# Kernel tuning notes

Hardware: AMD Instinct MI355X
Metric: run time of the kernel (lower is better)

Reference implementation:

```python
import jax, jax.numpy as jnp
import numpy as np

N_NODES = 100000
IN_DIM = 128
HID = 128
N_REL = 2
N_EDGES = 500000


def setup_inputs() -> dict:
    key = jax.random.key(0)
    ks = jax.random.split(key, 12)
    x = jax.random.normal(ks[0], (N_NODES, IN_DIM), dtype=jnp.float32)
    edge_index = jax.random.randint(ks[1], (2, N_EDGES), 0, N_NODES, dtype=jnp.int64)
    edge_type = jax.random.randint(ks[2], (N_EDGES,), 0, N_REL, dtype=jnp.int64)
    def w(k, shape, fan_in):
        return jax.random.normal(k, shape, dtype=jnp.float32) / np.sqrt(fan_in)
    return {
        "x": x,
        "edge_index": edge_index,
        "edge_type": edge_type,
        "W_rel1": w(ks[3], (N_REL, IN_DIM, HID), IN_DIM),
        "W_root1": w(ks[4], (IN_DIM, HID), IN_DIM),
        "b1": jnp.zeros((HID,), jnp.float32),
        "W_rel2": w(ks[5], (N_REL, HID, HID), HID),
        "W_root2": w(ks[6], (HID, HID), HID),
        "b2": jnp.zeros((HID,), jnp.float32),
        "Wc": w(ks[7], (HID, 2), HID),
        "bc": jnp.zeros((2,), jnp.float32),
    }


def rgcn_conv(x, src, dst, edge_type, W_rel, W_root, b, n_nodes):
    """PyG RGCNConv: out_i = x_i @ W_root + b + sum_r mean_{j in N_r(i)} x_j @ W_r."""
    out = x @ W_root + b
    for r in range(W_rel.shape[0]):  # small fixed relation count
        mask = (edge_type == r).astype(x.dtype)  # [E]
        xr = x @ W_rel[r]                         # [N, dout] transform-then-gather
        msg = xr[src] * mask[:, None]             # [E, dout]
        agg = jax.ops.segment_sum(msg, dst, num_segments=n_nodes)   # [N, dout]
        cnt = jax.ops.segment_sum(mask, dst, num_segments=n_nodes)  # [N]
        out = out + agg / jnp.maximum(cnt, 1.0)[:, None]            # mean aggr
    return out


def reference(x, edge_index, edge_type, W_rel1, W_root1, b1, W_rel2, W_root2, b2, Wc, bc):
    n = x.shape[0]
    src, dst = edge_index[0], edge_index[1]
    h = rgcn_conv(x, src, dst, edge_type, W_rel1, W_root1, b1, n)
    h = jax.nn.relu(h)
    # dropout is identity at inference (training=False)
    h = rgcn_conv(h, src, dst, edge_type, W_rel2, W_root2, b2, n)
    h = jax.nn.relu(h)
    logits = h @ Wc + bc
    return logits
```

## Files before the change

kernel.cpp:

```cpp
#include <hip/hip_runtime.h>
#include <hip/hip_fp16.h>

#define N_NODES 100000
#define PAD_N   100096
#define IN_DIM 128
#define HID 128
#define N_REL 2
#define N_EDGES 500000
#define M_SEG (N_REL * N_NODES)
#define SCAN_BLK 1024
#define SCAN_NB ((M_SEG + SCAN_BLK - 1) / SCAN_BLK)

#define CVT_BLOCKS 12500
#define PACK_BLOCKS 48
#define HIST_BLOCKS 1954

typedef __attribute__((ext_vector_type(8))) _Float16 half8;
typedef __attribute__((ext_vector_type(4))) float float4v;

__device__ __forceinline__ unsigned short f2h(float f) {
    return __half_as_ushort(__float2half(f));
}

__global__ __launch_bounds__(256) void prep_kernel(
    const float* __restrict__ X, unsigned short* __restrict__ Xb,
    const float* __restrict__ Wroot1, const float* __restrict__ Wrel1,
    const float* __restrict__ Wroot2, const float* __restrict__ Wrel2,
    unsigned short* __restrict__ Wp,
    const int* __restrict__ ei, const int* __restrict__ et,
    unsigned* __restrict__ cnt)
{
    int bid = blockIdx.x;
    if (bid < CVT_BLOCKS) {
        int i = bid * 256 + threadIdx.x;
        if (i >= N_NODES * IN_DIM / 4) return;
        float4 v = ((const float4*)X)[i];
        ushort4 o;
        o.x = f2h(v.x); o.y = f2h(v.y); o.z = f2h(v.z); o.w = f2h(v.w);
        ((ushort4*)Xb)[i] = o;
    } else if (bid < CVT_BLOCKS + PACK_BLOCKS) {
        int tid = (bid - CVT_BLOCKS) * 256 + threadIdx.x;
        int layer = tid / 6144;
        int rem   = tid % 6144;
        int ks    = rem / 512;
        int rem2  = rem % 512;
        int nt    = rem2 / 64;
        int lane  = rem2 % 64;
        int seg = ks >> 2;
        int kl  = (ks & 3) * 32 + (lane >> 4) * 8;
        int chan = nt * 16 + (lane & 15);
        const float* Wroot = layer ? Wroot2 : Wroot1;
        const float* Wrel  = layer ? Wrel2  : Wrel1;
        const float* W = (seg == 0) ? Wroot : (Wrel + (size_t)(seg - 1) * 128 * 128);
        unsigned short* dst = Wp + (size_t)tid * 8;
        #pragma unroll
        for (int j = 0; j < 8; ++j)
            dst[j] = f2h(W[(size_t)(kl + j) * 128 + chan]);
    } else {
        int e = (bid - CVT_BLOCKS - PACK_BLOCKS) * 256 + threadIdx.x;
        if (e >= N_EDGES) return;
        int dst = ei[N_EDGES + e];
        int r = et[e];
        atomicAdd(cnt + (size_t)r * N_NODES + dst, 1u);
    }
}

__global__ __launch_bounds__(256) void scan1_kernel(
    const unsigned* __restrict__ cnt,
    unsigned* __restrict__ rs, unsigned* __restrict__ bsums)
{
    __shared__ unsigned sdata[256];
    int t = threadIdx.x;
    int base = blockIdx.x * SCAN_BLK + t * 4;
    unsigned v[4]; unsigned s = 0;
    #pragma unroll
    for (int j = 0; j < 4; ++j) {
        v[j] = (base + j < M_SEG) ? cnt[base + j] : 0u;
        s += v[j];
    }
    sdata[t] = s;
    __syncthreads();
    #pragma unroll
    for (int off = 1; off < 256; off <<= 1) {
        unsigned x = (t >= off) ? sdata[t - off] : 0u;
        __syncthreads();
        if (t >= off) sdata[t] += x;
        __syncthreads();
    }
    unsigned excl = (t > 0) ? sdata[t - 1] : 0u;
    if (t == 255) bsums[blockIdx.x] = sdata[255];
    unsigned run = excl;
    #pragma unroll
    for (int j = 0; j < 4; ++j) {
        if (base + j < M_SEG) rs[base + j] = run;
        run += v[j];
    }
}

__global__ __launch_bounds__(256) void scan2_kernel(unsigned* __restrict__ bsums)
{
    __shared__ unsigned sdata[256];
    int t = threadIdx.x;
    sdata[t] = (t < SCAN_NB) ? bsums[t] : 0u;
    __syncthreads();
    #pragma unroll
    for (int off = 1; off < 256; off <<= 1) {
        unsigned x = (t >= off) ? sdata[t - off] : 0u;
        __syncthreads();
        if (t >= off) sdata[t] += x;
        __syncthreads();
    }
    if (t < SCAN_NB) bsums[t] = (t > 0) ? sdata[t - 1] : 0u;
}

__global__ __launch_bounds__(256) void scan3_kernel(
    unsigned* __restrict__ rs, const unsigned* __restrict__ bsums,
    unsigned* __restrict__ cursor)
{
    int i = blockIdx.x * blockDim.x + threadIdx.x;
    if (i < M_SEG) {
        unsigned v = rs[i] + bsums[i >> 10];
        rs[i] = v;
        cursor[i] = v;
    }
    if (i == 0) rs[M_SEG] = N_EDGES;
}

__global__ __launch_bounds__(256) void fill_kernel(
    const int* __restrict__ ei, const int* __restrict__ et,
    unsigned* __restrict__ cursor, unsigned* __restrict__ csr)
{
    int e = blockIdx.x * blockDim.x + threadIdx.x;
    if (e >= N_EDGES) return;
    int src = ei[e];
    int dst = ei[N_EDGES + e];
    int r = et[e];
    unsigned pos = atomicAdd(cursor + (size_t)r * N_NODES + dst, 1u);
    csr[pos] = (unsigned)src;
}

template <bool FINAL>
__global__ __launch_bounds__(256) void gemm_kernel(
    const unsigned short* __restrict__ Xin,
    const unsigned* __restrict__ rs,
    const unsigned* __restrict__ csr,
    const unsigned short* __restrict__ Wp,
    const float* __restrict__ bias,
    unsigned short* __restrict__ Hout,
    const float* __restrict__ Wc,
    const float* __restrict__ bc,
    float* __restrict__ Out)
{
    __shared__ unsigned short ldsB[2][3 * 8 * 512];

    const int t    = threadIdx.x;
    const int w    = t >> 6;
    const int lane = t & 63;
    const int l15  = lane & 15;
    const int quad = lane >> 4;
    const int rowbase = blockIdx.x * 128 + w * 32;
    const int koff = quad * 8;

    auto stage = [&](int ph, int buf) {
        #pragma unroll
        for (int fi = 0; fi < 6; ++fi) {
            int f  = fi * 4 + w;
            int sl = f >> 3;
            int nt = f & 7;
            int ks = ph * 3 + sl;
            const unsigned short* g = Wp + ((size_t)(ks * 8 + nt) * 64 + lane) * 8;
            unsigned short* l = &ldsB[buf][(size_t)(sl * 8 + nt) * 512];
            __builtin_amdgcn_global_load_lds(
                (const __attribute__((address_space(1))) unsigned int*)g,
                (__attribute__((address_space(3))) unsigned int*)l, 16, 0, 0);
        }
    };

    stage(0, 0);

    const uint4* __restrict__ X4 = (const uint4*)Xin;

    half8 ax[2][4];
    #pragma unroll
    for (int mt = 0; mt < 2; ++mt)
        #pragma unroll
        for (int ksl = 0; ksl < 4; ++ksl)
            ax[mt][ksl] = *(const half8*)(Xin +
                (size_t)(rowbase + mt * 16 + l15) * 128 + ksl * 32 + koff);

    half8 ag[2][2][4];
    #pragma unroll
    for (int r = 0; r < 2; ++r) {
        #pragma unroll
        for (int mt = 0; mt < 2; ++mt) {
            int node = rowbase + mt * 16 + l15;
            unsigned start = 0, end = 0;
            if (node < N_NODES) {
                unsigned sg = (unsigned)r * N_NODES + (unsigned)node;
                start = rs[sg];
                end   = rs[sg + 1];
            }
            __half2 a2[4][4];
            #pragma unroll
            for (int ksl = 0; ksl < 4; ++ksl)
                #pragma unroll
                for (int j = 0; j < 4; ++j)
                    a2[ksl][j] = __float2half2_rn(0.f);

            for (unsigned p = start; p < end; ++p) {
                unsigned s = csr[p];
                const uint4* row = X4 + ((size_t)s << 4) + quad;
                uint4 v0 = row[0];
                uint4 v1 = row[4];
                uint4 v2 = row[8];
                uint4 v3 = row[12];
                a2[0][0] = __hadd2(a2[0][0], *(const __half2*)&v0.x);
                a2[0][1] = __hadd2(a2[0][1], *(const __half2*)&v0.y);
                a2[0][2] = __hadd2(a2[0][2], *(const __half2*)&v0.z);
                a2[0][3] = __hadd2(a2[0][3], *(const __half2*)&v0.w);
                a2[1][0] = __hadd2(a2[1][0], *(const __half2*)&v1.x);
                a2[1][1] = __hadd2(a2[1][1], *(const __half2*)&v1.y);
                a2[1][2] = __hadd2(a2[1][2], *(const __half2*)&v1.z);
                a2[1][3] = __hadd2(a2[1][3], *(const __half2*)&v1.w);
                a2[2][0] = __hadd2(a2[2][0], *(const __half2*)&v2.x);
                a2[2][1] = __hadd2(a2[2][1], *(const __half2*)&v2.y);
                a2[2][2] = __hadd2(a2[2][2], *(const __half2*)&v2.z);
                a2[2][3] = __hadd2(a2[2][3], *(const __half2*)&v2.w);
                a2[3][0] = __hadd2(a2[3][0], *(const __half2*)&v3.x);
                a2[3][1] = __hadd2(a2[3][1], *(const __half2*)&v3.y);
                a2[3][2] = __hadd2(a2[3][2], *(const __half2*)&v3.z);
                a2[3][3] = __hadd2(a2[3][3], *(const __half2*)&v3.w);
            }

            unsigned c = end - start;
            float scf = 1.0f / (float)(c > 0u ? c : 1u);
            __half2 s2 = __float2half2_rn(scf);
            #pragma unroll
            for (int ksl = 0; ksl < 4; ++ksl) {
                half8 h;
                #pragma unroll
                for (int j = 0; j < 4; ++j)
                    ((__half2*)&h)[j] = __hmul2(a2[ksl][j], s2);
                ag[r][mt][ksl] = h;
            }
        }
    }

    auto af = [&](int ks, int mt) -> half8 {
        return (ks < 4) ? ax[mt][ks & 3] : ag[(ks >> 2) - 1][mt][ks & 3];
    };

    float4v acc[2][8];
    #pragma unroll
    for (int nt = 0; nt < 8; ++nt) {
        float bv = bias[nt * 16 + l15];
        #pragma unroll
        for (int mt = 0; mt < 2; ++mt)
            acc[mt][nt] = float4v{bv, bv, bv, bv};
    }

    __syncthreads();

    #pragma unroll
    for (int ph = 0; ph < 4; ++ph) {
        if (ph < 3) stage(ph + 1, (ph + 1) & 1);
        #pragma unroll
        for (int sl = 0; sl < 3; ++sl) {
            int ks = ph * 3 + sl;
            half8 b[8];
            #pragma unroll
            for (int nt = 0; nt < 8; ++nt)
                b[nt] = *(const half8*)(&ldsB[ph & 1][(size_t)(sl * 8 + nt) * 512] + lane * 8);
            #pragma unroll
            for (int nt = 0; nt < 8; ++nt) {
                acc[0][nt] = __builtin_amdgcn_mfma_f32_16x16x32_f16(af(ks, 0), b[nt], acc[0][nt], 0, 0, 0);
                acc[1][nt] = __builtin_amdgcn_mfma_f32_16x16x32_f16(af(ks, 1), b[nt], acc[1][nt], 0, 0, 0);
            }
        }
        __syncthreads();
    }

    if (!FINAL) {
        #pragma unroll
        for (int mt = 0; mt < 2; ++mt) {
            #pragma unroll
            for (int r = 0; r < 4; ++r) {
                int node = rowbase + mt * 16 + quad * 4 + r;
                unsigned short* hp = Hout + (size_t)node * 128 + l15;
                #pragma unroll
                for (int nt = 0; nt < 8; ++nt)
                    hp[nt * 16] = f2h(fmaxf(acc[mt][nt][r], 0.f));
            }
        }
    } else {
        float wc0[8], wc1[8];
        #pragma unroll
        for (int nt = 0; nt < 8; ++nt) {
            wc0[nt] = Wc[(nt * 16 + l15) * 2 + 0];
            wc1[nt] = Wc[(nt * 16 + l15) * 2 + 1];
        }
        float b0 = bc[0], b1 = bc[1];
        #pragma unroll
        for (int mt = 0; mt < 2; ++mt) {
            #pragma unroll
            for (int r = 0; r < 4; ++r) {
                float l0 = 0.f, l1 = 0.f;
                #pragma unroll
                for (int nt = 0; nt < 8; ++nt) {
                    float h = fmaxf(acc[mt][nt][r], 0.f);
                    l0 += h * wc0[nt];
                    l1 += h * wc1[nt];
                }
                #pragma unroll
                for (int off = 8; off > 0; off >>= 1) {
                    l0 += __shfl_down(l0, off, 16);
                    l1 += __shfl_down(l1, off, 16);
                }
                int node = rowbase + mt * 16 + quad * 4 + r;
                if (l15 == 0 && node < N_NODES) {
                    Out[(size_t)node * 2 + 0] = l0 + b0;
                    Out[(size_t)node * 2 + 1] = l1 + b1;
                }
            }
        }
    }
}

extern "C" void kernel_launch(void* const* d_in, const int* in_sizes, int n_in,
                              void* d_out, int out_size, void* d_ws, size_t ws_size,
                              hipStream_t stream)
{
    const float* x      = (const float*)d_in[0];
    const int*   ei     = (const int*)d_in[1];
    const int*   et     = (const int*)d_in[2];
    const float* Wrel1  = (const float*)d_in[3];
    const float* Wroot1 = (const float*)d_in[4];
    const float* b1     = (const float*)d_in[5];
    const float* Wrel2  = (const float*)d_in[6];
    const float* Wroot2 = (const float*)d_in[7];
    const float* b2     = (const float*)d_in[8];
    const float* Wc     = (const float*)d_in[9];
    const float* bc     = (const float*)d_in[10];
    float* out = (float*)d_out;

    char* ws = (char*)d_ws;
    size_t off = 0;
    auto alloc = [&](size_t bytes) {
        void* p = ws + off;
        off += (bytes + 255) & ~(size_t)255;
        return p;
    };
    unsigned short* xb    = (unsigned short*)alloc((size_t)PAD_N * IN_DIM * 2);
    unsigned short* h1b   = (unsigned short*)alloc((size_t)PAD_N * HID * 2);
    unsigned short* Wp    = (unsigned short*)alloc((size_t)2 * 12 * 8 * 64 * 8 * 2);
    unsigned*       rs    = (unsigned*)alloc((size_t)(M_SEG + 1) * 4);
    unsigned*       cursor= (unsigned*)alloc((size_t)M_SEG * 4);
    unsigned*       bsums = (unsigned*)alloc(256 * 4);
    unsigned*       csr   = (unsigned*)alloc((size_t)N_EDGES * 4);

    const int edge_blocks = (N_EDGES + 255) / 256;
    const int seg_blocks  = (M_SEG + 255) / 256;
    const int gemm_blocks = PAD_N / 128;
    const int prep_blocks = CVT_BLOCKS + PACK_BLOCKS + HIST_BLOCKS;

    hipMemsetAsync(cursor, 0, (size_t)M_SEG * 4, stream);
    prep_kernel<<<prep_blocks, 256, 0, stream>>>(
        x, xb, Wroot1, Wrel1, Wroot2, Wrel2, Wp, ei, et, cursor);
    scan1_kernel<<<SCAN_NB, 256, 0, stream>>>(cursor, rs, bsums);
    scan2_kernel<<<1, 256, 0, stream>>>(bsums);
    scan3_kernel<<<seg_blocks, 256, 0, stream>>>(rs, bsums, cursor);
    fill_kernel<<<edge_blocks, 256, 0, stream>>>(ei, et, cursor, csr);

    gemm_kernel<false><<<gemm_blocks, 256, 0, stream>>>(
        xb, rs, csr, Wp, b1, h1b, nullptr, nullptr, nullptr);

    gemm_kernel<true><<<gemm_blocks, 256, 0, stream>>>(
        h1b, rs, csr, Wp + (size_t)12 * 8 * 64 * 8, b2, nullptr, Wc, bc, out);
}
```

Before: 273.3 us.

## Interleave four neighbor gathers per lane and load weights directly from global

The neighbor aggregation now advances all four (relation, row-tile) segments together in one predicated loop. Each lane therefore issues four independent row gathers per iteration instead of walking each segment serially, which raises memory-level parallelism. The shared-memory staging of the weight matrix and its block barriers are removed; B and A fragments are loaded straight from global memory into registers with software double buffering. This frees LDS and drops the syncs, but adds register pressure and redundant global weight reads across waves, and masked iterations still issue gathers to row 0.

After: 271.3 us. No clear change (-0.7%).

```diff
diff --git a/kernel.cpp b/kernel.cpp
--- a/kernel.cpp
+++ b/kernel.cpp
@@ -151,8 +151,6 @@
     const float* __restrict__ bc,
     float* __restrict__ Out)
 {
-    __shared__ unsigned short ldsB[2][3 * 8 * 512];
-
     const int t    = threadIdx.x;
     const int w    = t >> 6;
     const int lane = t & 63;
@@ -161,93 +159,98 @@
     const int rowbase = blockIdx.x * 128 + w * 32;
     const int koff = quad * 8;
 
-    auto stage = [&](int ph, int buf) {
-        #pragma unroll
-        for (int fi = 0; fi < 6; ++fi) {
-            int f  = fi * 4 + w;
-            int sl = f >> 3;
-            int nt = f & 7;
-            int ks = ph * 3 + sl;
-            const unsigned short* g = Wp + ((size_t)(ks * 8 + nt) * 64 + lane) * 8;
-            unsigned short* l = &ldsB[buf][(size_t)(sl * 8 + nt) * 512];
-            __builtin_amdgcn_global_load_lds(
-                (const __attribute__((address_space(1))) unsigned int*)g,
-                (__attribute__((address_space(3))) unsigned int*)l, 16, 0, 0);
-        }
-    };
-
-    stage(0, 0);
-
     const uint4* __restrict__ X4 = (const uint4*)Xin;
 
-    half8 ax[2][4];
-    #pragma unroll
-    for (int mt = 0; mt < 2; ++mt)
-        #pragma unroll
-        for (int ksl = 0; ksl < 4; ++ksl)
-            ax[mt][ksl] = *(const half8*)(Xin +
-                (size_t)(rowbase + mt * 16 + l15) * 128 + ksl * 32 + koff);
-
-    half8 ag[2][2][4];
+    unsigned p_[4], e_[4]; float inv_[4];
     #pragma unroll
     for (int r = 0; r < 2; ++r) {
         #pragma unroll
         for (int mt = 0; mt < 2; ++mt) {
+            int c = r * 2 + mt;
             int node = rowbase + mt * 16 + l15;
-            unsigned start = 0, end = 0;
+            unsigned st = 0, en = 0;
             if (node < N_NODES) {
                 unsigned sg = (unsigned)r * N_NODES + (unsigned)node;
-                start = rs[sg];
-                end   = rs[sg + 1];
-            }
-            __half2 a2[4][4];
+                st = rs[sg];
+                en = rs[sg + 1];
+            }
+            p_[c] = st; e_[c] = en;
+            unsigned cdeg = en - st;
+            inv_[c] = 1.0f / (float)(cdeg > 0u ? cdeg : 1u);
+        }
+    }
+
+    __half2 a2[4][4][4];
+    #pragma unroll
+    for (int c = 0; c < 4; ++c)
+        #pragma unroll
+        for (int ksl = 0; ksl < 4; ++ksl)
+            #pragma unroll
+            for (int j = 0; j < 4; ++j)
+                a2[c][ksl][j] = __float2half2_rn(0.f);
+
+    const __half2 one2  = __float2half2_rn(1.f);
+    const __half2 zero2 = __float2half2_rn(0.f);
+
+    while (true) {
+        bool act[4];
+        bool anyl = false;
+        #pragma unroll
+        for (int c = 0; c < 4; ++c) { act[c] = p_[c] < e_[c]; anyl |= act[c]; }
+        if (!__any(anyl)) break;
+
+        unsigned s_[4];
+        #pragma unroll
+        for (int c = 0; c < 4; ++c)
+            s_[c] = csr[act[c] ? p_[c] : 0u];
+
+        uint4 v_[4][4];
+        #pragma unroll
+        for (int c = 0; c < 4; ++c) {
+            const uint4* row = X4 + ((size_t)(act[c] ? s_[c] : 0u) << 4) + quad;
+            v_[c][0] = row[0];
+            v_[c][1] = row[4];
+            v_[c][2] = row[8];
+            v_[c][3] = row[12];
+        }
+
+        #pragma unroll
+        for (int c = 0; c < 4; ++c) {
+            __half2 m = act[c] ? one2 : zero2;
             #pragma unroll
             for (int ksl = 0; ksl < 4; ++ksl)
                 #pragma unroll
                 for (int j = 0; j < 4; ++j)
-                    a2[ksl][j] = __float2half2_rn(0.f);
-
-            for (unsigned p = start; p < end; ++p) {
-                unsigned s = csr[p];
-                const uint4* row = X4 + ((size_t)s << 4) + quad;
-                uint4 v0 = row[0];
-                uint4 v1 = row[4];
-                uint4 v2 = row[8];
-                uint4 v3 = row[12];
-                a2[0][0] = __hadd2(a2[0][0], *(const __half2*)&v0.x);
-                a2[0][1] = __hadd2(a2[0][1], *(const __half2*)&v0.y);
-                a2[0][2] = __hadd2(a2[0][2], *(const __half2*)&v0.z);
-                a2[0][3] = __hadd2(a2[0][3], *(const __half2*)&v0.w);
-                a2[1][0] = __hadd2(a2[1][0], *(const __half2*)&v1.x);
-                a2[1][1] = __hadd2(a2[1][1], *(const __half2*)&v1.y);
-                a2[1][2] = __hadd2(a2[1][2], *(const __half2*)&v1.z);
-                a2[1][3] = __hadd2(a2[1][3], *(const __half2*)&v1.w);
-                a2[2][0] = __hadd2(a2[2][0], *(const __half2*)&v2.x);
-                a2[2][1] = __hadd2(a2[2][1], *(const __half2*)&v2.y);
-                a2[2][2] = __hadd2(a2[2][2], *(const __half2*)&v2.z);
-                a2[2][3] = __hadd2(a2[2][3], *(const __half2*)&v2.w);
-                a2[3][0] = __hadd2(a2[3][0], *(const __half2*)&v3.x);
-                a2[3][1] = __hadd2(a2[3][1], *(const __half2*)&v3.y);
-                a2[3][2] = __hadd2(a2[3][2], *(const __half2*)&v3.z);
-                a2[3][3] = __hadd2(a2[3][3], *(const __half2*)&v3.w);
-            }
-
-            unsigned c = end - start;
-            float scf = 1.0f / (float)(c > 0u ? c : 1u);
-            __half2 s2 = __float2half2_rn(scf);
+                    a2[c][ksl][j] = __hfma2(((const __half2*)&v_[c][ksl])[j], m,
+                                            a2[c][ksl][j]);
+            p_[c] += act[c] ? 1u : 0u;
+        }
+    }
+
+    half8 ag[2][2][4];
+    #pragma unroll
+    for (int r = 0; r < 2; ++r)
+        #pragma unroll
+        for (int mt = 0; mt < 2; ++mt) {
+            int c = r * 2 + mt;
+            __half2 s2 = __float2half2_rn(inv_[c]);
             #pragma unroll
             for (int ksl = 0; ksl < 4; ++ksl) {
                 half8 h;
                 #pragma unroll
                 for (int j = 0; j < 4; ++j)
-                    ((__half2*)&h)[j] = __hmul2(a2[ksl][j], s2);
+                    ((__half2*)&h)[j] = __hmul2(a2[c][ksl][j], s2);
                 ag[r][mt][ksl] = h;
             }
         }
-    }
-
-    auto af = [&](int ks, int mt) -> half8 {
-        return (ks < 4) ? ax[mt][ks & 3] : ag[(ks >> 2) - 1][mt][ks & 3];
+
+    auto ldB = [&](int ks, int nt) -> half8 {
+        return *(const half8*)(Wp + ((size_t)(ks * 8 + nt) * 64 + lane) * 8);
+    };
+    const unsigned short* aBase0 = Xin + (size_t)(rowbase + l15) * 128 + koff;
+    const unsigned short* aBase1 = aBase0 + 16 * 128;
+    auto ldA = [&](int ks, int mt) -> half8 {
+        return *(const half8*)((mt ? aBase1 : aBase0) + (ks & 3) * 32);
     };
 
     float4v acc[2][8];
@@ -259,25 +262,31 @@
             acc[mt][nt] = float4v{bv, bv, bv, bv};
     }
 
-    __syncthreads();
-
-    #pragma unroll
-    for (int ph = 0; ph < 4; ++ph) {
-        if (ph < 3) stage(ph + 1, (ph + 1) & 1);
-        #pragma unroll
-        for (int sl = 0; sl < 3; ++sl) {
-            int ks = ph * 3 + sl;
-            half8 b[8];
+    half8 bb[2][8];
+    half8 aa[2][2];
+    #pragma unroll
+    for (int nt = 0; nt < 8; ++nt) bb[0][nt] = ldB(0, nt);
+    aa[0][0] = ldA(0, 0);
+    aa[0][1] = ldA(0, 1);
+
+    #pragma unroll
+    for (int ks = 0; ks < 12; ++ks) {
+        if (ks + 1 < 12) {
             #pragma unroll
             for (int nt = 0; nt < 8; ++nt)
-                b[nt] = *(const half8*)(&ldsB[ph & 1][(size_t)(sl * 8 + nt) * 512] + lane * 8);
-            #pragma unroll
-            for (int nt = 0; nt < 8; ++nt) {
-                acc[0][nt] = __builtin_amdgcn_mfma_f32_16x16x32_f16(af(ks, 0), b[nt], acc[0][nt], 0, 0, 0);
-                acc[1][nt] = __builtin_amdgcn_mfma_f32_16x16x32_f16(af(ks, 1), b[nt], acc[1][nt], 0, 0, 0);
-            }
-        }
-        __syncthreads();
+                bb[(ks + 1) & 1][nt] = ldB(ks + 1, nt);
+            if (ks + 1 < 4) {
+                aa[(ks + 1) & 1][0] = ldA(ks + 1, 0);
+                aa[(ks + 1) & 1][1] = ldA(ks + 1, 1);
+            }
+        }
+        half8 A0 = (ks < 4) ? aa[ks & 1][0] : ag[(ks >> 2) - 1][0][ks & 3];
+        half8 A1 = (ks < 4) ? aa[ks & 1][1] : ag[(ks >> 2) - 1][1][ks & 3];
+        #pragma unroll
+        for (int nt = 0; nt < 8; ++nt) {
+            acc[0][nt] = __builtin_amdgcn_mfma_f32_16x16x32_f16(A0, bb[ks & 1][nt], acc[0][nt], 0, 0, 0);
+            acc[1][nt] = __builtin_amdgcn_mfma_f32_16x16x32_f16(A1, bb[ks & 1][nt], acc[1][nt], 0, 0, 0);
+        }
     }
 
     if (!FINAL) {
```
